# Kernel optimization log

Measured on AMD Instinct MI355X. Metric: run time of the kernel, lower is better.

Reference implementation:

```python
import jax, jax.numpy as jnp
import numpy as np

N = 100000   # total nodes
E = 1000000  # edges
D = 64       # input_dim
H = 128      # embed_dim


def setup_inputs() -> dict:
    key = jax.random.key(0)
    k1, k2, k3, k4 = jax.random.split(key, 4)
    nodes = jnp.arange(N, dtype=jnp.int32)
    features = jax.random.normal(k1, (N, D), dtype=jnp.float32)
    edge_index = jax.random.randint(k2, (2, E), 0, N, dtype=jnp.int32)
    # nn.Linear(2*D, H): weight [H, 2D], bias [H]
    W = jax.random.normal(k3, (H, 2 * D), dtype=jnp.float32) / np.sqrt(2 * D)
    b = jax.random.normal(k4, (H,), dtype=jnp.float32) * 0.01
    return {"nodes": nodes, "features": features, "edge_index": edge_index,
            "W": W, "b": b}


def reference(nodes, features, edge_index, W, b):
    src, dst = edge_index[0], edge_index[1]
    # gcn=False: neighbors are undirected (both src->dst and dst->src).
    # Mean aggregator over all neighbors (full-neighborhood mean).
    ones = jnp.ones((E,), dtype=features.dtype)
    neigh_sum = (jax.ops.segment_sum(features[dst], src, num_segments=N)
                 + jax.ops.segment_sum(features[src], dst, num_segments=N))
    deg = (jax.ops.segment_sum(ones, src, num_segments=N)
           + jax.ops.segment_sum(ones, dst, num_segments=N))
    neigh_mean = neigh_sum / jnp.maximum(deg, 1.0)[:, None]  # [N, D]
    self_feats = features[nodes]            # [B, D]
    neigh_feats = neigh_mean[nodes]         # [B, D]
    combined = jnp.concatenate([self_feats, neigh_feats], axis=1)  # [B, 2D]
    out = jax.nn.relu(combined @ W.T + b)   # [B, H]
    return out
```

## Files before the change

kernel.cpp:

```cpp
#include <hip/hip_runtime.h>
#include <hip/hip_bf16.h>


#define D_IN 64
#define H_OUT 128
#define CAP 64
#define CAP_L 61
#define NPB 32
#define BSHIFT 8
#define BUK_N 256
#define NBUK_MAX 512
#define PASSA_BLOCKS 256
#define PASSA_THREADS 512
#define OVF_CAP 32768

typedef unsigned long long ull;
typedef unsigned short ushortt;
typedef unsigned char uchar;
typedef __attribute__((ext_vector_type(8))) short bf16x8;
typedef __attribute__((ext_vector_type(4))) float f32x4;
typedef __attribute__((ext_vector_type(2))) float f32x2;

__device__ __forceinline__ ushortt f2bf(float f) {
    __hip_bfloat16 h = __float2bfloat16(f);
    return *reinterpret_cast<ushortt*>(&h);
}
__device__ __forceinline__ float bf2f(ushortt u) {
    unsigned int x = ((unsigned int)u) << 16;
    return __uint_as_float(x);
}

__global__ __launch_bounds__(PASSA_THREADS) void bucket_a_kernel(
    const int* __restrict__ ei,
    unsigned* __restrict__ gbuf,
    int* __restrict__ blkcnt,
    ull* __restrict__ ovf,
    int* __restrict__ ovfn,
    int E, int nbuk, int scap, int chunk)
{
    __shared__ int lcnt[NBUK_MAX];
    const int t = threadIdx.x;
    for (int i = t; i < nbuk; i += PASSA_THREADS) lcnt[i] = 0;
    __syncthreads();

    const int E2 = 2 * E;
    int lo = blockIdx.x * chunk;
    int hi = lo + chunk; if (hi > E2) hi = E2;

    for (int i = lo + t; i < hi; i += PASSA_THREADS) {
        int u = ei[i];
        int v = (i < E) ? ei[E + i] : ei[i - E];
        int b = u >> BSHIFT;
        unsigned pk = ((unsigned)v << BSHIFT) | (unsigned)(u & (BUK_N - 1));
        int p = atomicAdd(&lcnt[b], 1);
        if (p < scap) {
            gbuf[((size_t)blockIdx.x * nbuk + b) * scap + p] = pk;
        } else {
            int gp = atomicAdd(ovfn, 1);
            if (gp < OVF_CAP) ovf[gp] = ((ull)(unsigned)v << 32) | (unsigned)u;
        }
    }
    __syncthreads();
    for (int b = t; b < nbuk; b += PASSA_THREADS) {
        int c = lcnt[b];
        blkcnt[blockIdx.x * nbuk + b] = c < scap ? c : scap;
    }
}

__global__ __launch_bounds__(512) void adj_lds_kernel(
    const unsigned* __restrict__ gbuf,
    const int* __restrict__ blkcnt,
    const ull* __restrict__ ovf,
    const int* __restrict__ ovfn,
    int* __restrict__ cnt,
    int* __restrict__ adj,
    int N, int nbuk, int scap)
{
    __shared__ unsigned adj_l[BUK_N * CAP_L];
    __shared__ int cnt_l[BUK_N];
    __shared__ int scnt_l[PASSA_BLOCKS];

    const int b = blockIdx.x;
    const int t = threadIdx.x;

    if (t < BUK_N) cnt_l[t] = 0;
    if (t < PASSA_BLOCKS) scnt_l[t] = blkcnt[t * nbuk + b];
    __syncthreads();

    const int wv   = t >> 6;
    const int lane = t & 63;

    for (int seg = wv; seg < PASSA_BLOCKS; seg += 8) {
        int c = scnt_l[seg];
        const unsigned* base = gbuf + ((size_t)seg * nbuk + b) * scap;
        for (int i = lane; i < c; i += 64) {
            unsigned e = base[i];
            int ul = e & (BUK_N - 1);
            int v  = (int)(e >> BSHIFT);
            int p  = atomicAdd(&cnt_l[ul], 1);
            if (p < CAP_L) adj_l[ul * CAP_L + p] = (unsigned)v;
        }
    }
    __syncthreads();

    int novf = *ovfn; if (novf > OVF_CAP) novf = OVF_CAP;
    for (int i = t; i < novf; i += 512) {
        ull pk = ovf[i];
        int u = (int)(unsigned)(pk & 0xffffffffu);
        if ((u >> BSHIFT) == b) {
            int v = (int)(unsigned)(pk >> 32);
            int ul = u & (BUK_N - 1);
            int p  = atomicAdd(&cnt_l[ul], 1);
            if (p < CAP_L) adj_l[ul * CAP_L + p] = (unsigned)v;
        }
    }
    __syncthreads();

    if (t < BUK_N) {
        int g = (b << BSHIFT) + t;
        if (g < N) {
            int c = cnt_l[t];
            cnt[g] = c;
            int cl = c < CAP_L ? c : CAP_L;
            int k4 = (cl + 3) >> 2;
            for (int s = 0; s < k4; ++s) {
                uint4 o;
                o.x = adj_l[t * CAP_L + 4 * s + 0];
                o.y = adj_l[t * CAP_L + 4 * s + 1];
                o.z = adj_l[t * CAP_L + 4 * s + 2];
                o.w = adj_l[t * CAP_L + 4 * s + 3];
                *(uint4*)&adj[(size_t)g * CAP + 4 * s] = o;
            }
        }
    }
}

__global__ __launch_bounds__(256) void build_adj_kernel(
    const int* __restrict__ ei,
    int* __restrict__ cnt,
    int* __restrict__ adj,
    int E)
{
    const int part   = blockIdx.x & 7;
    const int bloc   = blockIdx.x >> 3;
    const int nbp    = gridDim.x >> 3;
    const int stride = nbp * 256;
    const int E2     = 2 * E;

    for (int i = bloc * 256 + (int)threadIdx.x; i < E2; i += stride) {
        int u = ei[i];
        if (((u >> 4) & 7) != part) continue;
        int v = (i < E) ? ei[E + i] : ei[i - E];
        int p = atomicAdd(&cnt[u], 1);
        if (p < CAP_L) adj[u * CAP + p] = v;
    }
}

__global__ __launch_bounds__(256) void convert_kernel(
    const float4* __restrict__ feat4,
    const float4* __restrict__ w4,
    ushortt* __restrict__ fb,
    uint2* __restrict__ fq,
    ushortt* __restrict__ Wb,
    int nfeat8, int nw8)
{
    int i = blockIdx.x * 256 + threadIdx.x;
    if (i < nfeat8) {
        float4 a = feat4[2 * i], b = feat4[2 * i + 1];
        bf16x8 o;
        o[0] = (short)f2bf(a.x); o[1] = (short)f2bf(a.y);
        o[2] = (short)f2bf(a.z); o[3] = (short)f2bf(a.w);
        o[4] = (short)f2bf(b.x); o[5] = (short)f2bf(b.y);
        o[6] = (short)f2bf(b.z); o[7] = (short)f2bf(b.w);
        *(bf16x8*)&fb[(size_t)i * 8] = o;
        unsigned lo = (unsigned)__builtin_amdgcn_cvt_pk_fp8_f32(a.x, a.y, 0, false);
        lo = (unsigned)__builtin_amdgcn_cvt_pk_fp8_f32(a.z, a.w, (int)lo, true);
        unsigned hi = (unsigned)__builtin_amdgcn_cvt_pk_fp8_f32(b.x, b.y, 0, false);
        hi = (unsigned)__builtin_amdgcn_cvt_pk_fp8_f32(b.z, b.w, (int)hi, true);
        uint2 q; q.x = lo; q.y = hi;
        fq[i] = q;
    } else {
        int j = i - nfeat8;
        if (j < nw8) {
            float4 a = w4[2 * j], b = w4[2 * j + 1];
            bf16x8 o;
            o[0] = (short)f2bf(a.x); o[1] = (short)f2bf(a.y);
            o[2] = (short)f2bf(a.z); o[3] = (short)f2bf(a.w);
            o[4] = (short)f2bf(b.x); o[5] = (short)f2bf(b.y);
            o[6] = (short)f2bf(b.z); o[7] = (short)f2bf(b.w);
            *(bf16x8*)&Wb[(size_t)j * 8] = o;
        }
    }
}

__global__ __launch_bounds__(256) void aggregate_fp8_kernel(
    const uchar* __restrict__ fq,
    int* __restrict__ adjmean,
    const int* __restrict__ cnt,
    int N)
{
    int wid  = (blockIdx.x * blockDim.x + threadIdx.x) >> 6;
    int lane = threadIdx.x & 63;
    if (wid >= N) return;

    const int oct = lane >> 3;
    const int ol  = lane & 7;

    int c  = cnt[wid];
    int cc = c < CAP_L ? c : CAP_L;

    int ids = 0;
    if (lane < cc) ids = adjmean[wid * CAP + lane];

    float s[8];
#pragma unroll
    for (int k = 0; k < 8; ++k) s[k] = 0.0f;

    for (int j = 0; j < cc; j += 16) {
        int j0 = j + oct;
        int j1 = j + 8 + oct;
        int a0 = j0 < cc;
        int a1 = j1 < cc;
        int id0 = __shfl(ids, a0 ? j0 : cc - 1);
        int id1 = __shfl(ids, a1 ? j1 : cc - 1);
        uint2 u0 = *(const uint2*)(fq + (size_t)id0 * 64 + ol * 8);
        uint2 u1 = *(const uint2*)(fq + (size_t)id1 * 64 + ol * 8);
        if (!a0) { u0.x = 0u; u0.y = 0u; }
        if (!a1) { u1.x = 0u; u1.y = 0u; }
        f32x2 p;
        p = __builtin_amdgcn_cvt_pk_f32_fp8((int)u0.x, false); s[0] += p.x; s[1] += p.y;
        p = __builtin_amdgcn_cvt_pk_f32_fp8((int)u0.x, true);  s[2] += p.x; s[3] += p.y;
        p = __builtin_amdgcn_cvt_pk_f32_fp8((int)u0.y, false); s[4] += p.x; s[5] += p.y;
        p = __builtin_amdgcn_cvt_pk_f32_fp8((int)u0.y, true);  s[6] += p.x; s[7] += p.y;
        p = __builtin_amdgcn_cvt_pk_f32_fp8((int)u1.x, false); s[0] += p.x; s[1] += p.y;
        p = __builtin_amdgcn_cvt_pk_f32_fp8((int)u1.x, true);  s[2] += p.x; s[3] += p.y;
        p = __builtin_amdgcn_cvt_pk_f32_fp8((int)u1.y, false); s[4] += p.x; s[5] += p.y;
        p = __builtin_amdgcn_cvt_pk_f32_fp8((int)u1.y, true);  s[6] += p.x; s[7] += p.y;
    }

#pragma unroll
    for (int m = 8; m <= 32; m <<= 1) {
#pragma unroll
        for (int k = 0; k < 8; ++k) s[k] += __shfl_xor(s[k], m);
    }

    if (oct == 0) {
        float r = 1.0f / fmaxf((float)c, 1.0f);
        bf16x8 o;
#pragma unroll
        for (int k = 0; k < 8; ++k) o[k] = (short)f2bf(s[k] * r);
        ushortt* mrow = (ushortt*)&adjmean[wid * CAP];
        *(bf16x8*)&mrow[ol * 8] = o;
    }
}

__global__ __launch_bounds__(256) void aggregate_bf16_kernel(
    const ushortt* __restrict__ fb,
    int* __restrict__ adjmean,
    const int* __restrict__ cnt,
    int N)
{
    int wid  = (blockIdx.x * blockDim.x + threadIdx.x) >> 6;
    int lane = threadIdx.x & 63;
    if (wid >= N) return;

    int c  = cnt[wid];
    int cc = c < CAP_L ? c : CAP_L;
    int ids = adjmean[wid * CAP + lane];

    float sum = 0.0f;
    int j = 0;
    for (; j + 8 <= cc; j += 8) {
        int i0 = __shfl(ids, j + 0);
        int i1 = __shfl(ids, j + 1);
        int i2 = __shfl(ids, j + 2);
        int i3 = __shfl(ids, j + 3);
        int i4 = __shfl(ids, j + 4);
        int i5 = __shfl(ids, j + 5);
        int i6 = __shfl(ids, j + 6);
        int i7 = __shfl(ids, j + 7);
        float f0 = bf2f(fb[i0 * D_IN + lane]);
        float f1 = bf2f(fb[i1 * D_IN + lane]);
        float f2 = bf2f(fb[i2 * D_IN + lane]);
        float f3 = bf2f(fb[i3 * D_IN + lane]);
        float f4 = bf2f(fb[i4 * D_IN + lane]);
        float f5 = bf2f(fb[i5 * D_IN + lane]);
        float f6 = bf2f(fb[i6 * D_IN + lane]);
        float f7 = bf2f(fb[i7 * D_IN + lane]);
        sum += ((f0 + f1) + (f2 + f3)) + ((f4 + f5) + (f6 + f7));
    }
    for (; j < cc; ++j)
        sum += bf2f(fb[__shfl(ids, j) * D_IN + lane]);

    float m = sum / fmaxf((float)c, 1.0f);
    ushortt* mrow = (ushortt*)&adjmean[wid * CAP];
    mrow[lane] = f2bf(m);
}

__global__ __launch_bounds__(256) void aggregate_f32_kernel(
    const float* __restrict__ feat,
    int* __restrict__ adjmean,
    const int* __restrict__ cnt,
    int N)
{
    int wid  = (blockIdx.x * blockDim.x + threadIdx.x) >> 6;
    int lane = threadIdx.x & 63;
    if (wid >= N) return;

    int c  = cnt[wid];
    int cc = c < CAP_L ? c : CAP_L;
    int ids = adjmean[wid * CAP + lane];

    float sum = 0.0f;
    int j = 0;
    for (; j + 8 <= cc; j += 8) {
        int i0 = __shfl(ids, j + 0);
        int i1 = __shfl(ids, j + 1);
        int i2 = __shfl(ids, j + 2);
        int i3 = __shfl(ids, j + 3);
        int i4 = __shfl(ids, j + 4);
        int i5 = __shfl(ids, j + 5);
        int i6 = __shfl(ids, j + 6);
        int i7 = __shfl(ids, j + 7);
        float f0 = feat[i0 * D_IN + lane];
        float f1 = feat[i1 * D_IN + lane];
        float f2 = feat[i2 * D_IN + lane];
        float f3 = feat[i3 * D_IN + lane];
        float f4 = feat[i4 * D_IN + lane];
        float f5 = feat[i5 * D_IN + lane];
        float f6 = feat[i6 * D_IN + lane];
        float f7 = feat[i7 * D_IN + lane];
        sum += ((f0 + f1) + (f2 + f3)) + ((f4 + f5) + (f6 + f7));
    }
    for (; j < cc; ++j)
        sum += feat[__shfl(ids, j) * D_IN + lane];

    float m = sum / fmaxf((float)c, 1.0f);
    ushortt* mrow = (ushortt*)&adjmean[wid * CAP];
    mrow[lane] = f2bf(m);
}

__global__ __launch_bounds__(256) void gemm_mfma_kernel(
    const int* __restrict__ nodes,
    const ushortt* __restrict__ fb,
    const ushortt* __restrict__ meanb,
    const ushortt* __restrict__ Wb,
    const float* __restrict__ bias,
    float* __restrict__ out,
    int N)
{
    __shared__ ushortt w_lds[128 * 136];
    __shared__ int gnode[64];

    const int t  = threadIdx.x;
    const int n0 = blockIdx.x * 64;

    if (t < 64) {
        int idx = n0 + t;
        gnode[t] = nodes[idx < N ? idx : N - 1];
    }
    for (int i = t; i < 128 * 16; i += 256) {
        int row = i >> 4, seg = i & 15;
        *(bf16x8*)&w_lds[row * 136 + seg * 8] =
            *(const bf16x8*)&Wb[row * 128 + seg * 8];
    }
    __syncthreads();

    const int w    = t >> 6;
    const int lane = t & 63;
    const int l15  = lane & 15;
    const int quad = lane >> 4;

    const int g = gnode[w * 16 + l15];
    const bf16x8 a0 = *(const bf16x8*)&fb[(size_t)g * D_IN +  0 + quad * 8];
    const bf16x8 a1 = *(const bf16x8*)&fb[(size_t)g * D_IN + 32 + quad * 8];
    const bf16x8 a2 = *(const bf16x8*)&meanb[(size_t)g * 128 +  0 + quad * 8];
    const bf16x8 a3 = *(const bf16x8*)&meanb[(size_t)g * 128 + 32 + quad * 8];

#pragma unroll
    for (int tile = 0; tile < 8; ++tile) {
        const int h0 = tile * 16;
        const ushortt* wrow = &w_lds[(h0 + l15) * 136];
        bf16x8 b0 = *(const bf16x8*)&wrow[ 0 + quad * 8];
        bf16x8 b1 = *(const bf16x8*)&wrow[32 + quad * 8];
        bf16x8 b2 = *(const bf16x8*)&wrow[64 + quad * 8];
        bf16x8 b3 = *(const bf16x8*)&wrow[96 + quad * 8];

        f32x4 acc = {0.f, 0.f, 0.f, 0.f};
        acc = __builtin_amdgcn_mfma_f32_16x16x32_bf16(a0, b0, acc, 0, 0, 0);
        acc = __builtin_amdgcn_mfma_f32_16x16x32_bf16(a1, b1, acc, 0, 0, 0);
        acc = __builtin_amdgcn_mfma_f32_16x16x32_bf16(a2, b2, acc, 0, 0, 0);
        acc = __builtin_amdgcn_mfma_f32_16x16x32_bf16(a3, b3, acc, 0, 0, 0);

        const float bh = bias[h0 + l15];
#pragma unroll
        for (int r = 0; r < 4; ++r) {
            int idx = n0 + w * 16 + quad * 4 + r;
            if (idx < N)
                out[(size_t)idx * H_OUT + h0 + l15] = fmaxf(acc[r] + bh, 0.0f);
        }
    }
}

__global__ __launch_bounds__(256) void gemm_kernel(
    const int* __restrict__ nodes,
    const float* __restrict__ feat,
    const ushortt* __restrict__ meanb,
    const float* __restrict__ W,
    const float* __restrict__ bias,
    float* __restrict__ out,
    int N)
{
    __shared__ float w_lds[64 * 132];
    __shared__ float comb_self[NPB * 68];
    __shared__ float comb_mean[NPB * 68];
    __shared__ int   gnode[NPB];

    const int t  = threadIdx.x;
    const int n0 = blockIdx.x * NPB;

    if (t < NPB) {
        int idx = n0 + t;
        if (idx >= N) idx = N - 1;
        gnode[t] = nodes[idx];
    }
    __syncthreads();

    for (int i = t; i < NPB * 64; i += 256) {
        int n = i >> 6, d = i & 63;
        int g = gnode[n];
        comb_self[n * 68 + d] = feat[g * D_IN + d];
        comb_mean[n * 68 + d] = bf2f(meanb[(size_t)g * 128 + d]);
    }
    for (int i = t; i < H_OUT * 64; i += 256) {
        int h = i >> 6, kk = i & 63;
        w_lds[kk * 132 + h] = W[h * (2 * D_IN) + kk];
    }
    __syncthreads();

    const int tx = t & 31;
    const int ty = t >> 5;
    const int h0 = tx * 4;
    const int nl = ty * 4;

    float acc[4][4];
#pragma unroll
    for (int j = 0; j < 4; j++)
#pragma unroll
        for (int i = 0; i < 4; i++) acc[j][i] = 0.0f;

    for (int kk = 0; kk < 64; kk += 4) {
        float4 wvv[4], cv[4];
#pragma unroll
        for (int i = 0; i < 4; i++)
            wvv[i] = *(const float4*)&w_lds[(kk + i) * 132 + h0];
#pragma unroll
        for (int j = 0; j < 4; j++)
            cv[j] = *(const float4*)&comb_self[(nl + j) * 68 + kk];
#pragma unroll
        for (int j = 0; j < 4; j++) {
            const float* c = (const float*)&cv[j];
#pragma unroll
            for (int i = 0; i < 4; i++) {
                const float* wp = (const float*)&wvv[i];
                acc[j][0] += wp[0] * c[i];
                acc[j][1] += wp[1] * c[i];
                acc[j][2] += wp[2] * c[i];
                acc[j][3] += wp[3] * c[i];
            }
        }
    }
    __syncthreads();

    for (int i = t; i < H_OUT * 64; i += 256) {
        int h = i >> 6, kk = i & 63;
        w_lds[kk * 132 + h] = W[h * (2 * D_IN) + 64 + kk];
    }
    __syncthreads();

    for (int kk = 0; kk < 64; kk += 4) {
        float4 wvv[4], cv[4];
#pragma unroll
        for (int i = 0; i < 4; i++)
            wvv[i] = *(const float4*)&w_lds[(kk + i) * 132 + h0];
#pragma unroll
        for (int j = 0; j < 4; j++)
            cv[j] = *(const float4*)&comb_mean[(nl + j) * 68 + kk];
#pragma unroll
        for (int j = 0; j < 4; j++) {
            const float* c = (const float*)&cv[j];
#pragma unroll
            for (int i = 0; i < 4; i++) {
                const float* wp = (const float*)&wvv[i];
                acc[j][0] += wp[0] * c[i];
                acc[j][1] += wp[1] * c[i];
                acc[j][2] += wp[2] * c[i];
                acc[j][3] += wp[3] * c[i];
            }
        }
    }

    float4 bv = *(const float4*)&bias[h0];
#pragma unroll
    for (int j = 0; j < 4; j++) {
        int n = n0 + nl + j;
        if (n >= N) continue;
        float4 o;
        o.x = fmaxf(acc[j][0] + bv.x, 0.0f);
        o.y = fmaxf(acc[j][1] + bv.y, 0.0f);
        o.z = fmaxf(acc[j][2] + bv.z, 0.0f);
        o.w = fmaxf(acc[j][3] + bv.w, 0.0f);
        *(float4*)&out[(size_t)n * H_OUT + h0] = o;
    }
}

extern "C" void kernel_launch(void* const* d_in, const int* in_sizes, int n_in,
                              void* d_out, int out_size, void* d_ws, size_t ws_size,
                              hipStream_t stream) {
    const int*   nodes = (const int*)d_in[0];
    const float* feat  = (const float*)d_in[1];
    const int*   ei    = (const int*)d_in[2];
    const float* W     = (const float*)d_in[3];
    const float* bias  = (const float*)d_in[4];
    float*       out   = (float*)d_out;

    const int N  = in_sizes[0];
    const int E  = in_sizes[2] / 2;
    const int E2 = 2 * E;

    const int nbuk  = (N + BUK_N - 1) >> BSHIFT;
    const int chunk = (E2 + PASSA_BLOCKS - 1) / PASSA_BLOCKS;
    double ex = (double)chunk * (double)BUK_N / (double)N;
    int scap = ((int)(ex + 5.0 * __builtin_sqrt(ex)) + 31) & ~15;

    char* base = (char*)d_ws;
    size_t off = 0;
    auto aln = [](size_t x) { return (x + 63) & ~(size_t)63; };
    int* cnt      = (int*)(base + off); off = aln(off + (size_t)N * 4);
    int* ovfn     = (int*)(base + off); off = aln(off + 64);
    int* adjmean  = (int*)(base + off); off = aln(off + (size_t)N * CAP * 4);
    int* blkcnt   = (int*)(base + off); off = aln(off + (size_t)PASSA_BLOCKS * NBUK_MAX * 4);
    ull* ovf      = (ull*)(base + off); off = aln(off + (size_t)OVF_CAP * 8);
    ushortt* Wb   = (ushortt*)(base + off); off = aln(off + (size_t)H_OUT * 2 * D_IN * 2);
    char* big     = base + off;
    unsigned* gbuf = (unsigned*)big;
    ushortt*  fb   = (ushortt*)big;
    uchar*    fq   = (uchar*)(fb + (size_t)N * D_IN);

    const size_t gbuf_b  = (size_t)PASSA_BLOCKS * nbuk * scap * 4;
    const size_t fb_b    = (size_t)N * D_IN * 2;
    const size_t fq_b    = (size_t)N * D_IN;
    const size_t big_mfma = (gbuf_b > fb_b + fq_b ? gbuf_b : fb_b + fq_b);
    const size_t big_old  = (gbuf_b > fb_b ? gbuf_b : fb_b);

    const bool use_new  = (N <= 131072) && (nbuk <= NBUK_MAX)
                        && (ws_size >= off + big_old);
    const bool use_bf16 = (ws_size >= off + big_old);
    const bool use_mfma = use_new && (ws_size >= off + big_mfma);

    if (use_new) {
        hipMemsetAsync(ovfn, 0, 16 * sizeof(int), stream);
        bucket_a_kernel<<<PASSA_BLOCKS, PASSA_THREADS, 0, stream>>>(
            ei, gbuf, blkcnt, ovf, ovfn, E, nbuk, scap, chunk);
        adj_lds_kernel<<<nbuk, 512, 0, stream>>>(gbuf, blkcnt, ovf, ovfn,
                                                 cnt, adjmean, N, nbuk, scap);
    } else {
        hipMemsetAsync(cnt, 0, (size_t)N * sizeof(int), stream);
        hipMemsetAsync(ovfn, 0, 16 * sizeof(int), stream);
        build_adj_kernel<<<2048, 256, 0, stream>>>(ei, cnt, adjmean, E);
    }

    const int ablocks = (int)(((size_t)N * 64 + 255) / 256);
    const int n4f = N * D_IN / 4;

    if (use_mfma) {
        const int nfeat8 = N * D_IN / 8;
        const int nw8    = H_OUT * 2 * D_IN / 8;
        convert_kernel<<<(nfeat8 + nw8 + 255) / 256, 256, 0, stream>>>(
            (const float4*)feat, (const float4*)W, fb, (uint2*)fq, Wb,
            nfeat8, nw8);
        aggregate_fp8_kernel<<<ablocks, 256, 0, stream>>>(fq, adjmean, cnt, N);
        gemm_mfma_kernel<<<(N + 63) / 64, 256, 0, stream>>>(
            nodes, fb, (const ushortt*)adjmean, Wb, bias, out, N);
    } else {
        if (use_bf16) {
            convert_kernel<<<(N * D_IN / 8 + 255) / 256, 256, 0, stream>>>(
                (const float4*)feat, (const float4*)W, fb, (uint2*)fq, Wb,
                N * D_IN / 8, 0);
            aggregate_bf16_kernel<<<ablocks, 256, 0, stream>>>(fb, adjmean,
                                                               cnt, N);
        } else {
            aggregate_f32_kernel<<<ablocks, 256, 0, stream>>>(feat, adjmean,
                                                              cnt, N);
        }
        gemm_kernel<<<(N + NPB - 1) / NPB, 256, 0, stream>>>(
            nodes, feat, (const ushortt*)adjmean, W, bias, out, N);
    }
}
```

Measured before the change: 195.1 us.

## Separate compact mean buffer, fold overflow reset into convert, vectorize GEMM output stores

```diff
diff --git a/kernel.cpp b/kernel.cpp
--- a/kernel.cpp
+++ b/kernel.cpp
@@ -162,8 +162,10 @@
     ushortt* __restrict__ fb,
     uint2* __restrict__ fq,
     ushortt* __restrict__ Wb,
+    int* __restrict__ ovfn,
     int nfeat8, int nw8)
 {
+    if (blockIdx.x == 0 && threadIdx.x == 0) *ovfn = 0;
     int i = blockIdx.x * 256 + threadIdx.x;
     if (i < nfeat8) {
         float4 a = feat4[2 * i], b = feat4[2 * i + 1];
@@ -195,8 +197,9 @@
 
 __global__ __launch_bounds__(256) void aggregate_fp8_kernel(
     const uchar* __restrict__ fq,
-    int* __restrict__ adjmean,
+    const int* __restrict__ adj,
     const int* __restrict__ cnt,
+    ushortt* __restrict__ meanb,
     int N)
 {
     int wid  = (blockIdx.x * blockDim.x + threadIdx.x) >> 6;
@@ -210,54 +213,66 @@
     int cc = c < CAP_L ? c : CAP_L;
 
     int ids = 0;
-    if (lane < cc) ids = adjmean[wid * CAP + lane];
-
-    float s[8];
-#pragma unroll
-    for (int k = 0; k < 8; ++k) s[k] = 0.0f;
-
-    for (int j = 0; j < cc; j += 16) {
+    if (lane < cc) ids = adj[wid * CAP + lane];
+
+    f32x2 s0 = {0.f, 0.f}, s1 = {0.f, 0.f}, s2 = {0.f, 0.f}, s3 = {0.f, 0.f};
+
+    int j = 0;
+    for (; j + 8 < cc; j += 16) {
         int j0 = j + oct;
         int j1 = j + 8 + oct;
-        int a0 = j0 < cc;
         int a1 = j1 < cc;
-        int id0 = __shfl(ids, a0 ? j0 : cc - 1);
+        int id0 = __shfl(ids, j0);
         int id1 = __shfl(ids, a1 ? j1 : cc - 1);
         uint2 u0 = *(const uint2*)(fq + (size_t)id0 * 64 + ol * 8);
         uint2 u1 = *(const uint2*)(fq + (size_t)id1 * 64 + ol * 8);
+        if (!a1) { u1.x = 0u; u1.y = 0u; }
+        s0 += __builtin_amdgcn_cvt_pk_f32_fp8((int)u0.x, false);
+        s1 += __builtin_amdgcn_cvt_pk_f32_fp8((int)u0.x, true);
+        s2 += __builtin_amdgcn_cvt_pk_f32_fp8((int)u0.y, false);
+        s3 += __builtin_amdgcn_cvt_pk_f32_fp8((int)u0.y, true);
+        s0 += __builtin_amdgcn_cvt_pk_f32_fp8((int)u1.x, false);
+        s1 += __builtin_amdgcn_cvt_pk_f32_fp8((int)u1.x, true);
+        s2 += __builtin_amdgcn_cvt_pk_f32_fp8((int)u1.y, false);
+        s3 += __builtin_amdgcn_cvt_pk_f32_fp8((int)u1.y, true);
+    }
+    if (j < cc) {
+        int j0 = j + oct;
+        int a0 = j0 < cc;
+        int id0 = __shfl(ids, a0 ? j0 : cc - 1);
+        uint2 u0 = *(const uint2*)(fq + (size_t)id0 * 64 + ol * 8);
         if (!a0) { u0.x = 0u; u0.y = 0u; }
-        if (!a1) { u1.x = 0u; u1.y = 0u; }
-        f32x2 p;
-        p = __builtin_amdgcn_cvt_pk_f32_fp8((int)u0.x, false); s[0] += p.x; s[1] += p.y;
-        p = __builtin_amdgcn_cvt_pk_f32_fp8((int)u0.x, true);  s[2] += p.x; s[3] += p.y;
-        p = __builtin_amdgcn_cvt_pk_f32_fp8((int)u0.y, false); s[4] += p.x; s[5] += p.y;
-        p = __builtin_amdgcn_cvt_pk_f32_fp8((int)u0.y, true);  s[6] += p.x; s[7] += p.y;
-        p = __builtin_amdgcn_cvt_pk_f32_fp8((int)u1.x, false); s[0] += p.x; s[1] += p.y;
-        p = __builtin_amdgcn_cvt_pk_f32_fp8((int)u1.x, true);  s[2] += p.x; s[3] += p.y;
-        p = __builtin_amdgcn_cvt_pk_f32_fp8((int)u1.y, false); s[4] += p.x; s[5] += p.y;
-        p = __builtin_amdgcn_cvt_pk_f32_fp8((int)u1.y, true);  s[6] += p.x; s[7] += p.y;
+        s0 += __builtin_amdgcn_cvt_pk_f32_fp8((int)u0.x, false);
+        s1 += __builtin_amdgcn_cvt_pk_f32_fp8((int)u0.x, true);
+        s2 += __builtin_amdgcn_cvt_pk_f32_fp8((int)u0.y, false);
+        s3 += __builtin_amdgcn_cvt_pk_f32_fp8((int)u0.y, true);
     }
 
 #pragma unroll
     for (int m = 8; m <= 32; m <<= 1) {
-#pragma unroll
-        for (int k = 0; k < 8; ++k) s[k] += __shfl_xor(s[k], m);
+        f32x2 t;
+        t.x = __shfl_xor(s0.x, m); t.y = __shfl_xor(s0.y, m); s0 += t;
+        t.x = __shfl_xor(s1.x, m); t.y = __shfl_xor(s1.y, m); s1 += t;
+        t.x = __shfl_xor(s2.x, m); t.y = __shfl_xor(s2.y, m); s2 += t;
+        t.x = __shfl_xor(s3.x, m); t.y = __shfl_xor(s3.y, m); s3 += t;
     }
 
     if (oct == 0) {
         float r = 1.0f / fmaxf((float)c, 1.0f);
         bf16x8 o;
-#pragma unroll
-        for (int k = 0; k < 8; ++k) o[k] = (short)f2bf(s[k] * r);
-        ushortt* mrow = (ushortt*)&adjmean[wid * CAP];
-        *(bf16x8*)&mrow[ol * 8] = o;
-    }
-}
-
-__global__ __launch_bounds__(256) void aggregate_bf16_kernel(
-    const ushortt* __restrict__ fb,
-    int* __restrict__ adjmean,
+        o[0] = (short)f2bf(s0.x * r); o[1] = (short)f2bf(s0.y * r);
+        o[2] = (short)f2bf(s1.x * r); o[3] = (short)f2bf(s1.y * r);
+        o[4] = (short)f2bf(s2.x * r); o[5] = (short)f2bf(s2.y * r);
+        o[6] = (short)f2bf(s3.x * r); o[7] = (short)f2bf(s3.y * r);
+        *(bf16x8*)&meanb[(size_t)wid * D_IN + ol * 8] = o;
+    }
+}
+
+__global__ __launch_bounds__(256) void aggregate_f32_kernel(
+    const float* __restrict__ feat,
+    const int* __restrict__ adj,
     const int* __restrict__ cnt,
+    ushortt* __restrict__ meanb,
     int N)
 {
     int wid  = (blockIdx.x * blockDim.x + threadIdx.x) >> 6;
@@ -266,50 +281,7 @@
 
     int c  = cnt[wid];
     int cc = c < CAP_L ? c : CAP_L;
-    int ids = adjmean[wid * CAP + lane];
-
-    float sum = 0.0f;
-    int j = 0;
-    for (; j + 8 <= cc; j += 8) {
-        int i0 = __shfl(ids, j + 0);
-        int i1 = __shfl(ids, j + 1);
-        int i2 = __shfl(ids, j + 2);
-        int i3 = __shfl(ids, j + 3);
-        int i4 = __shfl(ids, j + 4);
-        int i5 = __shfl(ids, j + 5);
-        int i6 = __shfl(ids, j + 6);
-        int i7 = __shfl(ids, j + 7);
-        float f0 = bf2f(fb[i0 * D_IN + lane]);
-        float f1 = bf2f(fb[i1 * D_IN + lane]);
-        float f2 = bf2f(fb[i2 * D_IN + lane]);
-        float f3 = bf2f(fb[i3 * D_IN + lane]);
-        float f4 = bf2f(fb[i4 * D_IN + lane]);
-        float f5 = bf2f(fb[i5 * D_IN + lane]);
-        float f6 = bf2f(fb[i6 * D_IN + lane]);
-        float f7 = bf2f(fb[i7 * D_IN + lane]);
-        sum += ((f0 + f1) + (f2 + f3)) + ((f4 + f5) + (f6 + f7));
-    }
-    for (; j < cc; ++j)
-        sum += bf2f(fb[__shfl(ids, j) * D_IN + lane]);
-
-    float m = sum / fmaxf((float)c, 1.0f);
-    ushortt* mrow = (ushortt*)&adjmean[wid * CAP];
-    mrow[lane] = f2bf(m);
-}
-
-__global__ __launch_bounds__(256) void aggregate_f32_kernel(
-    const float* __restrict__ feat,
-    int* __restrict__ adjmean,
-    const int* __restrict__ cnt,
-    int N)
-{
-    int wid  = (blockIdx.x * blockDim.x + threadIdx.x) >> 6;
-    int lane = threadIdx.x & 63;
-    if (wid >= N) return;
-
-    int c  = cnt[wid];
-    int cc = c < CAP_L ? c : CAP_L;
-    int ids = adjmean[wid * CAP + lane];
+    int ids = adj[wid * CAP + lane];
 
     float sum = 0.0f;
     int j = 0;
@@ -336,8 +308,7 @@
         sum += feat[__shfl(ids, j) * D_IN + lane];
 
     float m = sum / fmaxf((float)c, 1.0f);
-    ushortt* mrow = (ushortt*)&adjmean[wid * CAP];
-    mrow[lane] = f2bf(m);
+    meanb[(size_t)wid * D_IN + lane] = f2bf(m);
 }
 
 __global__ __launch_bounds__(256) void gemm_mfma_kernel(
@@ -374,8 +345,11 @@
     const int g = gnode[w * 16 + l15];
     const bf16x8 a0 = *(const bf16x8*)&fb[(size_t)g * D_IN +  0 + quad * 8];
     const bf16x8 a1 = *(const bf16x8*)&fb[(size_t)g * D_IN + 32 + quad * 8];
-    const bf16x8 a2 = *(const bf16x8*)&meanb[(size_t)g * 128 +  0 + quad * 8];
-    const bf16x8 a3 = *(const bf16x8*)&meanb[(size_t)g * 128 + 32 + quad * 8];
+    const bf16x8 a2 = *(const bf16x8*)&meanb[(size_t)g * D_IN +  0 + quad * 8];
+    const bf16x8 a3 = *(const bf16x8*)&meanb[(size_t)g * D_IN + 32 + quad * 8];
+
+    const int  out_row = n0 + w * 16 + l15;
+    const bool valid   = out_row < N;
 
 #pragma unroll
     for (int tile = 0; tile < 8; ++tile) {
@@ -387,17 +361,19 @@
         bf16x8 b3 = *(const bf16x8*)&wrow[96 + quad * 8];
 
         f32x4 acc = {0.f, 0.f, 0.f, 0.f};
-        acc = __builtin_amdgcn_mfma_f32_16x16x32_bf16(a0, b0, acc, 0, 0, 0);
-        acc = __builtin_amdgcn_mfma_f32_16x16x32_bf16(a1, b1, acc, 0, 0, 0);
-        acc = __builtin_amdgcn_mfma_f32_16x16x32_bf16(a2, b2, acc, 0, 0, 0);
-        acc = __builtin_amdgcn_mfma_f32_16x16x32_bf16(a3, b3, acc, 0, 0, 0);
-
-        const float bh = bias[h0 + l15];
-#pragma unroll
-        for (int r = 0; r < 4; ++r) {
-            int idx = n0 + w * 16 + quad * 4 + r;
-            if (idx < N)
-                out[(size_t)idx * H_OUT + h0 + l15] = fmaxf(acc[r] + bh, 0.0f);
+        acc = __builtin_amdgcn_mfma_f32_16x16x32_bf16(b0, a0, acc, 0, 0, 0);
+        acc = __builtin_amdgcn_mfma_f32_16x16x32_bf16(b1, a1, acc, 0, 0, 0);
+        acc = __builtin_amdgcn_mfma_f32_16x16x32_bf16(b2, a2, acc, 0, 0, 0);
+        acc = __builtin_amdgcn_mfma_f32_16x16x32_bf16(b3, a3, acc, 0, 0, 0);
+
+        if (valid) {
+            float4 bv = *(const float4*)&bias[h0 + quad * 4];
+            float4 o;
+            o.x = fmaxf(acc[0] + bv.x, 0.0f);
+            o.y = fmaxf(acc[1] + bv.y, 0.0f);
+            o.z = fmaxf(acc[2] + bv.z, 0.0f);
+            o.w = fmaxf(acc[3] + bv.w, 0.0f);
+            *(float4*)&out[(size_t)out_row * H_OUT + h0 + quad * 4] = o;
         }
     }
 }
@@ -430,7 +406,7 @@
         int n = i >> 6, d = i & 63;
         int g = gnode[n];
         comb_self[n * 68 + d] = feat[g * D_IN + d];
-        comb_mean[n * 68 + d] = bf2f(meanb[(size_t)g * 128 + d]);
+        comb_mean[n * 68 + d] = bf2f(meanb[(size_t)g * D_IN + d]);
     }
     for (int i = t; i < H_OUT * 64; i += 256) {
         int h = i >> 6, kk = i & 63;
@@ -536,64 +512,45 @@
     char* base = (char*)d_ws;
     size_t off = 0;
     auto aln = [](size_t x) { return (x + 63) & ~(size_t)63; };
-    int* cnt      = (int*)(base + off); off = aln(off + (size_t)N * 4);
-    int* ovfn     = (int*)(base + off); off = aln(off + 64);
-    int* adjmean  = (int*)(base + off); off = aln(off + (size_t)N * CAP * 4);
-    int* blkcnt   = (int*)(base + off); off = aln(off + (size_t)PASSA_BLOCKS * NBUK_MAX * 4);
-    ull* ovf      = (ull*)(base + off); off = aln(off + (size_t)OVF_CAP * 8);
-    ushortt* Wb   = (ushortt*)(base + off); off = aln(off + (size_t)H_OUT * 2 * D_IN * 2);
-    char* big     = base + off;
-    unsigned* gbuf = (unsigned*)big;
-    ushortt*  fb   = (ushortt*)big;
-    uchar*    fq   = (uchar*)(fb + (size_t)N * D_IN);
-
-    const size_t gbuf_b  = (size_t)PASSA_BLOCKS * nbuk * scap * 4;
-    const size_t fb_b    = (size_t)N * D_IN * 2;
-    const size_t fq_b    = (size_t)N * D_IN;
-    const size_t big_mfma = (gbuf_b > fb_b + fq_b ? gbuf_b : fb_b + fq_b);
-    const size_t big_old  = (gbuf_b > fb_b ? gbuf_b : fb_b);
-
-    const bool use_new  = (N <= 131072) && (nbuk <= NBUK_MAX)
-                        && (ws_size >= off + big_old);
-    const bool use_bf16 = (ws_size >= off + big_old);
-    const bool use_mfma = use_new && (ws_size >= off + big_mfma);
-
-    if (use_new) {
-        hipMemsetAsync(ovfn, 0, 16 * sizeof(int), stream);
+    int*     cnt    = (int*)(base + off);     off = aln(off + (size_t)N * 4);
+    int*     ovfn   = (int*)(base + off);     off = aln(off + 64);
+    int*     adj    = (int*)(base + off);     off = aln(off + (size_t)N * CAP * 4);
+    ushortt* meanb  = (ushortt*)(base + off); off = aln(off + (size_t)N * D_IN * 2);
+    const size_t off_min = off;
+    int*     blkcnt = (int*)(base + off);     off = aln(off + (size_t)PASSA_BLOCKS * NBUK_MAX * 4);
+    ull*     ovf    = (ull*)(base + off);     off = aln(off + (size_t)OVF_CAP * 8);
+    ushortt* Wb     = (ushortt*)(base + off); off = aln(off + (size_t)H_OUT * 2 * D_IN * 2);
+    ushortt* fb     = (ushortt*)(base + off); off = aln(off + (size_t)N * D_IN * 2);
+    uchar*   fq     = (uchar*)(base + off);   off = aln(off + (size_t)N * D_IN);
+    unsigned* gbuf  = (unsigned*)(base + off);
+    const size_t total = off + (size_t)PASSA_BLOCKS * nbuk * scap * 4;
+
+    const bool full = (N <= 131072) && (nbuk <= NBUK_MAX) && (ws_size >= total)
+                   && ((N * D_IN) % 8 == 0);
+
+    const int ablocks = (int)(((size_t)N * 64 + 255) / 256);
+
+    if (full) {
+        const int nfeat8 = N * D_IN / 8;
+        const int nw8    = H_OUT * 2 * D_IN / 8;
+        convert_kernel<<<(nfeat8 + nw8 + 255) / 256, 256, 0, stream>>>(
+            (const float4*)feat, (const float4*)W, fb, (uint2*)fq, Wb, ovfn,
+            nfeat8, nw8);
         bucket_a_kernel<<<PASSA_BLOCKS, PASSA_THREADS, 0, stream>>>(
             ei, gbuf, blkcnt, ovf, ovfn, E, nbuk, scap, chunk);
         adj_lds_kernel<<<nbuk, 512, 0, stream>>>(gbuf, blkcnt, ovf, ovfn,
-                                                 cnt, adjmean, N, nbuk, scap);
+                                                 cnt, adj, N, nbuk, scap);
+        aggregate_fp8_kernel<<<ablocks, 256, 0, stream>>>(fq, adj, cnt,
+                                                          meanb, N);
+        gemm_mfma_kernel<<<(N + 63) / 64, 256, 0, stream>>>(
+            nodes, fb, meanb, Wb, bias, out, N);
     } else {
+        (void)off_min;
         hipMemsetAsync(cnt, 0, (size_t)N * sizeof(int), stream);
-        hipMemsetAsync(ovfn, 0, 16 * sizeof(int), stream);
-        build_adj_kernel<<<2048, 256, 0, stream>>>(ei, cnt, adjmean, E);
-    }
-
-    const int ablocks = (int)(((size_t)N * 64 + 255) / 256);
-    const int n4f = N * D_IN / 4;
-
-    if (use_mfma) {
-        const int nfeat8 = N * D_IN / 8;
-        const int nw8    = H_OUT * 2 * D_IN / 8;
-        convert_kernel<<<(nfeat8 + nw8 + 255) / 256, 256, 0, stream>>>(
-            (const float4*)feat, (const float4*)W, fb, (uint2*)fq, Wb,
-            nfeat8, nw8);
-        aggregate_fp8_kernel<<<ablocks, 256, 0, stream>>>(fq, adjmean, cnt, N);
-        gemm_mfma_kernel<<<(N + 63) / 64, 256, 0, stream>>>(
-            nodes, fb, (const ushortt*)adjmean, Wb, bias, out, N);
-    } else {
-        if (use_bf16) {
-            convert_kernel<<<(N * D_IN / 8 + 255) / 256, 256, 0, stream>>>(
-                (const float4*)feat, (const float4*)W, fb, (uint2*)fq, Wb,
-                N * D_IN / 8, 0);
-            aggregate_bf16_kernel<<<ablocks, 256, 0, stream>>>(fb, adjmean,
-                                                               cnt, N);
-        } else {
-            aggregate_f32_kernel<<<ablocks, 256, 0, stream>>>(feat, adjmean,
-                                                              cnt, N);
-        }
+        build_adj_kernel<<<2048, 256, 0, stream>>>(ei, cnt, adj, E);
+        aggregate_f32_kernel<<<ablocks, 256, 0, stream>>>(feat, adj, cnt,
+                                                          meanb, N);
         gemm_kernel<<<(N + NPB - 1) / NPB, 256, 0, stream>>>(
-            nodes, feat, (const ushortt*)adjmean, W, bias, out, N);
-    }
-}
+            nodes, feat, meanb, W, bias, out, N);
+    }
+}
```

Result: no change. 192.9 us (-1.1%).
